# Kernel optimization log

Hardware: AMD Instinct MI355X
Metric: run time of the kernel (lower is better)

The kernel has to match this reference:

```python
import jax, jax.numpy as jnp
import numpy as np

B, L, IN_DIM = 4, 1024, 46
D, DS, K, EXP, NL = 256, 64, 4, 2, 4
DI = EXP * D            # 512 d_inner
HD = 64                 # ssm headdim
H = DI // HD            # 8 ssm heads
XBC = DI + 2 * DS       # 640 conv channels
DIP = 2 * DI + 2 * DS + H  # 1160 in_proj out dim
DFF = D * EXP           # 512 GatedMLP hidden
AH = 4                  # attn heads
AHD = D // AH           # 64


def setup_inputs() -> dict:
    key = jax.random.key(0)
    ks = iter(jax.random.split(key, 40))
    def rn(shape, s=0.05):
        return jax.random.normal(next(ks), shape, jnp.float32) * s
    return {
        'x': jax.random.normal(next(ks), (B, L, IN_DIM), jnp.float32),
        'pos_emb': rn((1, L, D), 0.02),
        'in_w': rn((IN_DIM, D)), 'in_b': jnp.zeros((D,), jnp.float32),
        'ln1_w': jnp.ones((NL, D), jnp.float32), 'ln1_b': jnp.zeros((NL, D), jnp.float32),
        'ssm_in_w': rn((NL, D, DIP)),
        'ssm_conv_w': rn((NL, K, XBC), 0.1), 'ssm_conv_b': jnp.zeros((NL, XBC), jnp.float32),
        'ssm_dt_bias': jnp.full((NL, H), -4.0, jnp.float32),
        'ssm_A_log': jnp.log(jnp.tile(jnp.arange(1.0, H + 1.0), (NL, 1))).astype(jnp.float32),
        'ssm_D': jnp.ones((NL, H), jnp.float32),
        'ssm_norm_w': jnp.ones((NL, DI), jnp.float32),
        'ssm_out_w': rn((NL, DI, D)),
        'ln2_w': jnp.ones((NL, D), jnp.float32), 'ln2_b': jnp.zeros((NL, D), jnp.float32),
        'fc1_w': rn((NL, D, 2 * DFF)), 'fc1_b': jnp.zeros((NL, 2 * DFF), jnp.float32),
        'fc2_w': rn((NL, DFF, D)), 'fc2_b': jnp.zeros((NL, D), jnp.float32),
        'attn_ln_w': jnp.ones((2, D), jnp.float32), 'attn_ln_b': jnp.zeros((2, D), jnp.float32),
        'attn_qkv_w': rn((2, D, 3 * D)), 'attn_qkv_b': jnp.zeros((2, 3 * D), jnp.float32),
        'attn_out_w': rn((2, D, D)), 'attn_out_b': jnp.zeros((2, D), jnp.float32),
        'norm_w': jnp.ones((D,), jnp.float32), 'norm_b': jnp.zeros((D,), jnp.float32),
        'dir_w': rn((D, 3)), 'dir_b': jnp.zeros((3,), jnp.float32),
        'reg_w': rn((D, 3)), 'reg_b': jnp.zeros((3,), jnp.float32),
    }


def _ln(x, w, b, eps=1e-5):
    m = jnp.mean(x, -1, keepdims=True)
    v = jnp.mean(jnp.square(x - m), -1, keepdims=True)
    return (x - m) * jax.lax.rsqrt(v + eps) * w + b


def _mamba2(h, in_w, conv_w, conv_b, dt_bias, A_log, Dh, nw, out_w):
    Bb, Ls, _ = h.shape
    zxbcdt = h @ in_w                               # [B,L,1160]
    z = zxbcdt[..., :DI]
    xBC = zxbcdt[..., DI:DI + XBC]
    dt = zxbcdt[..., DI + XBC:]                     # [B,L,H]
    # causal depthwise conv1d, kernel K
    xp = jnp.pad(xBC, ((0, 0), (K - 1, 0), (0, 0)))
    xBC = sum(xp[:, k:k + Ls, :] * conv_w[k] for k in range(K)) + conv_b
    xBC = jax.nn.silu(xBC)
    xs = xBC[..., :DI]
    Bm = xBC[..., DI:DI + DS]                       # [B,L,N]
    Cm = xBC[..., DI + DS:]                         # [B,L,N]
    dt = jax.nn.softplus(dt + dt_bias)              # [B,L,H]
    a = dt * (-jnp.exp(A_log))                      # [B,L,H], log-decay per step
    cA = jnp.cumsum(a, axis=1).transpose(0, 2, 1)   # [B,H,L]
    diff = cA[:, :, :, None] - cA[:, :, None, :]    # [B,H,L,L]
    mask = jnp.tril(jnp.ones((Ls, Ls), bool))
    decay = jnp.exp(jnp.where(mask, diff, -jnp.inf))
    CB = jnp.einsum('btn,bsn->bts', Cm, Bm)         # [B,L,L]
    S = decay * CB[:, None] * dt.transpose(0, 2, 1)[:, :, None, :]  # [B,H,L,L]
    x4 = xs.reshape(Bb, Ls, H, HD)
    y = jnp.einsum('bhts,bshp->bthp', S, x4) + Dh[None, None, :, None] * x4
    y = y.reshape(Bb, Ls, DI)
    y = y * jax.nn.silu(z)                          # gated
    y = y * jax.lax.rsqrt(jnp.mean(y * y, -1, keepdims=True) + 1e-5) * nw  # RMSNorm
    return y @ out_w


def _attn(h, qkv_w, qkv_b, out_w, out_b):
    Bb, Ls, _ = h.shape
    qkv = h @ qkv_w + qkv_b
    q, k, v = jnp.split(qkv, 3, axis=-1)
    q = q.reshape(Bb, Ls, AH, AHD).transpose(0, 2, 1, 3)
    k = k.reshape(Bb, Ls, AH, AHD).transpose(0, 2, 1, 3)
    v = v.reshape(Bb, Ls, AH, AHD).transpose(0, 2, 1, 3)
    scores = jnp.einsum('bhtd,bhsd->bhts', q, k) / np.sqrt(AHD).astype(np.float32)
    p = jax.nn.softmax(scores, axis=-1)
    o = jnp.einsum('bhts,bhsd->bhtd', p, v).transpose(0, 2, 1, 3).reshape(Bb, Ls, D)
    return o @ out_w + out_b


def _gmlp(h, w1, b1, w2, b2):
    x1, x2 = jnp.split(h @ w1 + b1, 2, axis=-1)
    return (jax.nn.gelu(x1, approximate=False) * x2) @ w2 + b2


def _forward(x, pos_emb, in_w, in_b, ln1_w, ln1_b, ssm_in_w, ssm_conv_w, ssm_conv_b,
             ssm_dt_bias, ssm_A_log, ssm_D, ssm_norm_w, ssm_out_w, ln2_w, ln2_b,
             fc1_w, fc1_b, fc2_w, fc2_b, attn_ln_w, attn_ln_b, attn_qkv_w, attn_qkv_b,
             attn_out_w, attn_out_b, norm_w, norm_b, dir_w, dir_b, reg_w, reg_b):
    Ls = x.shape[1]
    h = x @ in_w + in_b + pos_emb[:, :Ls, :]
    for i in range(NL):
        h = h + _mamba2(_ln(h, ln1_w[i], ln1_b[i]), ssm_in_w[i], ssm_conv_w[i],
                        ssm_conv_b[i], ssm_dt_bias[i], ssm_A_log[i], ssm_D[i],
                        ssm_norm_w[i], ssm_out_w[i])
        if i % 2 == 1:
            j = i // 2
            h = h + _attn(_ln(h, attn_ln_w[j], attn_ln_b[j]), attn_qkv_w[j],
                          attn_qkv_b[j], attn_out_w[j], attn_out_b[j])
        h = h + _gmlp(_ln(h, ln2_w[i], ln2_b[i]), fc1_w[i], fc1_b[i], fc2_w[i], fc2_b[i])
    h = _ln(h, norm_w, norm_b)
    hm = jnp.mean(h, axis=1)                        # [B, D]
    return hm @ dir_w + dir_b, hm @ reg_w + reg_b


def reference(x, pos_emb, in_w, in_b, ln1_w, ln1_b, ssm_in_w, ssm_conv_w, ssm_conv_b,
              ssm_dt_bias, ssm_A_log, ssm_D, ssm_norm_w, ssm_out_w, ln2_w, ln2_b,
              fc1_w, fc1_b, fc2_w, fc2_b, attn_ln_w, attn_ln_b, attn_qkv_w, attn_qkv_b,
              attn_out_w, attn_out_b, norm_w, norm_b, dir_w, dir_b, reg_w, reg_b):
    return _forward(x, pos_emb, in_w, in_b, ln1_w, ln1_b, ssm_in_w, ssm_conv_w,
                    ssm_conv_b, ssm_dt_bias, ssm_A_log, ssm_D, ssm_norm_w, ssm_out_w,
                    ln2_w, ln2_b, fc1_w, fc1_b, fc2_w, fc2_b, attn_ln_w, attn_ln_b,
                    attn_qkv_w, attn_qkv_b, attn_out_w, attn_out_b, norm_w, norm_b,
                    dir_w, dir_b, reg_w, reg_b)
```

## Files before the change

### kernel.cpp

```cpp
#include <hip/hip_runtime.h>
#include <math.h>

#define B_ 4
#define L_ 1024
#define IN_DIM_ 46
#define D_ 256
#define DS_ 64
#define K_ 4
#define NL_ 4
#define DI_ 512
#define HD_ 64
#define H_ 8
#define XBC_ 640
#define DIP_ 1160
#define DFF_ 512
#define AH_ 4
#define AHD_ 64
#define NT_ (B_*L_)
#define QKVD_ (3*D_)

__device__ __forceinline__ float block_sum_256(float v) {
    __shared__ float sb[4];
    #pragma unroll
    for (int off = 32; off > 0; off >>= 1) v += __shfl_down(v, off, 64);
    int lane = threadIdx.x & 63, wid = threadIdx.x >> 6;
    if (lane == 0) sb[wid] = v;
    __syncthreads();
    float r = sb[0] + sb[1] + sb[2] + sb[3];
    __syncthreads();
    return r;
}

__device__ __forceinline__ float siluf(float x) { return x / (1.f + expf(-x)); }
__device__ __forceinline__ float softplusf(float x) {
    return (x > 20.f) ? x : log1pf(expf(x));
}

__global__ __launch_bounds__(256) void in_proj_kernel(
        const float* __restrict__ x, const float* __restrict__ in_w,
        const float* __restrict__ in_b, const float* __restrict__ pos,
        float* __restrict__ Hb) {
    int t = blockIdx.x, tid = threadIdx.x;
    int l = t % L_;
    __shared__ float xs[IN_DIM_];
    if (tid < IN_DIM_) xs[tid] = x[(size_t)t * IN_DIM_ + tid];
    __syncthreads();
    float acc = in_b[tid] + pos[(size_t)l * D_ + tid];
    #pragma unroll 2
    for (int c = 0; c < IN_DIM_; ++c) acc += xs[c] * in_w[c * D_ + tid];
    Hb[(size_t)t * D_ + tid] = acc;
}

__global__ __launch_bounds__(256) void ln_kernel(
        const float* __restrict__ in, const float* __restrict__ w,
        const float* __restrict__ b, float* __restrict__ out) {
    int r = blockIdx.x, tid = threadIdx.x;
    float v = in[(size_t)r * D_ + tid];
    float mean = block_sum_256(v) * (1.f / D_);
    float c = v - mean;
    float var = block_sum_256(c * c) * (1.f / D_);
    out[(size_t)r * D_ + tid] = c * rsqrtf(var + 1e-5f) * w[tid] + b[tid];
}

template<bool BIAS, bool RES>
__global__ __launch_bounds__(256) void gemm64(
        const float* __restrict__ A, const float* __restrict__ W,
        const float* __restrict__ bias, const float* __restrict__ res,
        float* __restrict__ C, int M, int N, int Kd) {
    __shared__ __align__(16) float As[32][68];
    __shared__ __align__(16) float Ws[32][68];
    int tid = threadIdx.x;
    int tx = tid & 15, ty = tid >> 4;
    int n0 = blockIdx.x * 64, m0 = blockIdx.y * 64;
    float acc[4][4] = {};
    for (int k0 = 0; k0 < Kd; k0 += 32) {
        {
            int k = tid & 31, m = tid >> 5;
            #pragma unroll
            for (int i = 0; i < 8; ++i)
                As[k][m + i * 8] = A[(size_t)(m0 + m + i * 8) * Kd + k0 + k];
        }
        {
            #pragma unroll
            for (int i = 0; i < 2; ++i) {
                int idx = tid + i * 256;
                int k = idx >> 4, nq = idx & 15;
                int n = n0 + nq * 4;
                float4 wv;
                if (n + 3 < N) {
                    wv = *(const float4*)&W[(size_t)(k0 + k) * N + n];
                } else {
                    wv.x = (n + 0 < N) ? W[(size_t)(k0 + k) * N + n + 0] : 0.f;
                    wv.y = (n + 1 < N) ? W[(size_t)(k0 + k) * N + n + 1] : 0.f;
                    wv.z = (n + 2 < N) ? W[(size_t)(k0 + k) * N + n + 2] : 0.f;
                    wv.w = (n + 3 < N) ? W[(size_t)(k0 + k) * N + n + 3] : 0.f;
                }
                *(float4*)&Ws[k][nq * 4] = wv;
            }
        }
        __syncthreads();
        #pragma unroll
        for (int k = 0; k < 32; ++k) {
            float4 a  = *(const float4*)&As[k][ty * 4];
            float4 bb = *(const float4*)&Ws[k][tx * 4];
            acc[0][0] += a.x * bb.x; acc[0][1] += a.x * bb.y; acc[0][2] += a.x * bb.z; acc[0][3] += a.x * bb.w;
            acc[1][0] += a.y * bb.x; acc[1][1] += a.y * bb.y; acc[1][2] += a.y * bb.z; acc[1][3] += a.y * bb.w;
            acc[2][0] += a.z * bb.x; acc[2][1] += a.z * bb.y; acc[2][2] += a.z * bb.z; acc[2][3] += a.z * bb.w;
            acc[3][0] += a.w * bb.x; acc[3][1] += a.w * bb.y; acc[3][2] += a.w * bb.z; acc[3][3] += a.w * bb.w;
        }
        __syncthreads();
    }
    #pragma unroll
    for (int i = 0; i < 4; ++i) {
        int m = m0 + ty * 4 + i;
        int n = n0 + tx * 4;
        if (n + 3 < N) {
            float4 v = {acc[i][0], acc[i][1], acc[i][2], acc[i][3]};
            if (BIAS) {
                float4 bv = *(const float4*)&bias[n];
                v.x += bv.x; v.y += bv.y; v.z += bv.z; v.w += bv.w;
            }
            if (RES) {
                float4 rv = *(const float4*)&res[(size_t)m * N + n];
                v.x += rv.x; v.y += rv.y; v.z += rv.z; v.w += rv.w;
            }
            *(float4*)&C[(size_t)m * N + n] = v;
        } else {
            #pragma unroll
            for (int j = 0; j < 4; ++j) {
                int nn = n + j;
                if (nn < N) {
                    float v = acc[i][j];
                    if (BIAS) v += bias[nn];
                    if (RES) v += res[(size_t)m * N + nn];
                    C[(size_t)m * N + nn] = v;
                }
            }
        }
    }
}

__global__ __launch_bounds__(256) void conv_kernel(
        const float* __restrict__ ZX, const float* __restrict__ cw,
        const float* __restrict__ cb, float* __restrict__ XC) {
    int idx = blockIdx.x * 256 + threadIdx.x;
    if (idx >= NT_ * XBC_) return;
    int c = idx % XBC_;
    int t = idx / XBC_;
    int l = t % L_;
    float acc = cb[c];
    #pragma unroll
    for (int k = 0; k < K_; ++k) {
        int lp = l + k - (K_ - 1);
        if (lp >= 0)
            acc += ZX[(size_t)(t + k - (K_ - 1)) * DIP_ + DI_ + c] * cw[k * XBC_ + c];
    }
    XC[(size_t)idx] = siluf(acc);
}

__global__ __launch_bounds__(256) void dt_cumsum_kernel(
        const float* __restrict__ ZX, const float* __restrict__ dt_bias,
        const float* __restrict__ A_log, float* __restrict__ DT,
        float* __restrict__ CA) {
    int b = blockIdx.x / H_, h = blockIdx.x % H_;
    int tid = threadIdx.x;
    __shared__ float sc[256];
    float nA = -expf(A_log[h]);
    float bias = dt_bias[h];
    float carry = 0.f;
    for (int chunk = 0; chunk < L_ / 256; ++chunk) {
        int l = chunk * 256 + tid;
        size_t t = (size_t)b * L_ + l;
        float xv = ZX[t * DIP_ + DI_ + XBC_ + h] + bias;
        float dts = softplusf(xv);
        DT[t * H_ + h] = dts;
        float a = dts * nA;
        sc[tid] = a;
        __syncthreads();
        float v = a;
        for (int off = 1; off < 256; off <<= 1) {
            float add = (tid >= off) ? sc[tid - off] : 0.f;
            __syncthreads();
            v += add;
            sc[tid] = v;
            __syncthreads();
        }
        CA[t * H_ + h] = carry + v;
        carry += sc[255];
        __syncthreads();
    }
}

__global__ __launch_bounds__(256) void cb_kernel(
        const float* __restrict__ XC, float* __restrict__ CB) {
    int b = blockIdx.z;
    int t0 = blockIdx.y * 64, s0 = blockIdx.x * 64;
    if (s0 > t0 + 63) return;
    __shared__ __align__(16) float Cst[64][68];
    __shared__ __align__(16) float Bst[64][68];
    int tid = threadIdx.x, tx = tid & 15, ty = tid >> 4;
    {
        int dq = tid & 15, rr = tid >> 4;
        #pragma unroll
        for (int i = 0; i < 4; ++i) {
            int r2 = rr + i * 16;
            float4 cv = *(const float4*)&XC[(size_t)(b * L_ + t0 + r2) * XBC_ + DI_ + DS_ + dq * 4];
            Cst[dq * 4 + 0][r2] = cv.x; Cst[dq * 4 + 1][r2] = cv.y;
            Cst[dq * 4 + 2][r2] = cv.z; Cst[dq * 4 + 3][r2] = cv.w;
            float4 bv = *(const float4*)&XC[(size_t)(b * L_ + s0 + r2) * XBC_ + DI_ + dq * 4];
            Bst[dq * 4 + 0][r2] = bv.x; Bst[dq * 4 + 1][r2] = bv.y;
            Bst[dq * 4 + 2][r2] = bv.z; Bst[dq * 4 + 3][r2] = bv.w;
        }
    }
    __syncthreads();
    float acc[4][4] = {};
    #pragma unroll 4
    for (int n = 0; n < 64; ++n) {
        float4 a  = *(const float4*)&Cst[n][ty * 4];
        float4 bb = *(const float4*)&Bst[n][tx * 4];
        acc[0][0] += a.x * bb.x; acc[0][1] += a.x * bb.y; acc[0][2] += a.x * bb.z; acc[0][3] += a.x * bb.w;
        acc[1][0] += a.y * bb.x; acc[1][1] += a.y * bb.y; acc[1][2] += a.y * bb.z; acc[1][3] += a.y * bb.w;
        acc[2][0] += a.z * bb.x; acc[2][1] += a.z * bb.y; acc[2][2] += a.z * bb.z; acc[2][3] += a.z * bb.w;
        acc[3][0] += a.w * bb.x; acc[3][1] += a.w * bb.y; acc[3][2] += a.w * bb.z; acc[3][3] += a.w * bb.w;
    }
    #pragma unroll
    for (int i = 0; i < 4; ++i) {
        int t = t0 + ty * 4 + i;
        float4 v = {acc[i][0], acc[i][1], acc[i][2], acc[i][3]};
        *(float4*)&CB[((size_t)b * L_ + t) * L_ + s0 + tx * 4] = v;
    }
}

__global__ __launch_bounds__(256) void ssm_quad_kernel(
        const float* __restrict__ XC, const float* __restrict__ CB,
        const float* __restrict__ DT, const float* __restrict__ CA,
        const float* __restrict__ Dh_ptr, float* __restrict__ Y) {
    int b = blockIdx.z, h = blockIdx.y;
    int t0 = blockIdx.x * 64;
    int tid = threadIdx.x, tx = tid & 15, ty = tid >> 4;
    __shared__ __align__(16) float Pt[64][68];
    __shared__ __align__(16) float Xs[64][68];
    __shared__ float cat[64], cas[64], dts[64];
    if (tid < 64) cat[tid] = CA[((size_t)b * L_ + t0 + tid) * H_ + h];
    float acc[4][4] = {};
    float Dh = Dh_ptr[h];
    for (int s0 = 0; s0 <= t0; s0 += 64) {
        {
            int dq = tid & 15, rr = tid >> 4;
            #pragma unroll
            for (int i = 0; i < 4; ++i) {
                int ss = rr + i * 16;
                *(float4*)&Xs[ss][dq * 4] =
                    *(const float4*)&XC[(size_t)(b * L_ + s0 + ss) * XBC_ + h * HD_ + dq * 4];
            }
        }
        if (tid < 64) {
            cas[tid] = CA[((size_t)b * L_ + s0 + tid) * H_ + h];
            dts[tid] = DT[((size_t)b * L_ + s0 + tid) * H_ + h];
        }
        __syncthreads();
        bool diag = (s0 == t0);
        float p[4][4];
        #pragma unroll
        for (int i = 0; i < 4; ++i) {
            int t = ty * 4 + i;
            float ct = cat[t];
            float4 cbv = *(const float4*)&CB[((size_t)b * L_ + t0 + t) * L_ + s0 + tx * 4];
            float cb4[4] = {cbv.x, cbv.y, cbv.z, cbv.w};
            #pragma unroll
            for (int j = 0; j < 4; ++j) {
                int s = tx * 4 + j;
                float v = expf(ct - cas[s]) * cb4[j] * dts[s];
                if (diag && s > t) v = 0.f;
                p[i][j] = v;
            }
        }
        #pragma unroll
        for (int j = 0; j < 4; ++j) {
            float4 col = {p[0][j], p[1][j], p[2][j], p[3][j]};
            *(float4*)&Pt[tx * 4 + j][ty * 4] = col;
        }
        __syncthreads();
        #pragma unroll 4
        for (int s = 0; s < 64; ++s) {
            float4 a  = *(const float4*)&Pt[s][ty * 4];
            float4 xv = *(const float4*)&Xs[s][tx * 4];
            acc[0][0] += a.x * xv.x; acc[0][1] += a.x * xv.y; acc[0][2] += a.x * xv.z; acc[0][3] += a.x * xv.w;
            acc[1][0] += a.y * xv.x; acc[1][1] += a.y * xv.y; acc[1][2] += a.y * xv.z; acc[1][3] += a.y * xv.w;
            acc[2][0] += a.z * xv.x; acc[2][1] += a.z * xv.y; acc[2][2] += a.z * xv.z; acc[2][3] += a.z * xv.w;
            acc[3][0] += a.w * xv.x; acc[3][1] += a.w * xv.y; acc[3][2] += a.w * xv.z; acc[3][3] += a.w * xv.w;
        }
        __syncthreads();
    }
    #pragma unroll
    for (int i = 0; i < 4; ++i) {
        size_t t = (size_t)b * L_ + t0 + ty * 4 + i;
        float4 x4 = *(const float4*)&XC[t * XBC_ + h * HD_ + tx * 4];
        float4 o = {acc[i][0] + Dh * x4.x, acc[i][1] + Dh * x4.y,
                    acc[i][2] + Dh * x4.z, acc[i][3] + Dh * x4.w};
        *(float4*)&Y[t * DI_ + h * HD_ + tx * 4] = o;
    }
}

__global__ __launch_bounds__(256) void gate_rms_kernel(
        float* __restrict__ Y, const float* __restrict__ ZX,
        const float* __restrict__ nw) {
    int r = blockIdx.x, tid = threadIdx.x;
    size_t ry = (size_t)r * DI_, rz = (size_t)r * DIP_;
    float y0 = Y[ry + tid], y1 = Y[ry + 256 + tid];
    float z0 = ZX[rz + tid], z1 = ZX[rz + 256 + tid];
    y0 *= siluf(z0);
    y1 *= siluf(z1);
    float ss = block_sum_256(y0 * y0 + y1 * y1) * (1.f / DI_);
    float s = rsqrtf(ss + 1e-5f);
    Y[ry + tid] = y0 * s * nw[tid];
    Y[ry + 256 + tid] = y1 * s * nw[256 + tid];
}

__global__ __launch_bounds__(256) void attn_kernel(
        const float* __restrict__ QKV, float* __restrict__ O) {
    int b = blockIdx.z, hh = blockIdx.y;
    int t0 = blockIdx.x * 32;
    int tid = threadIdx.x, tx = tid & 15, ty = tid >> 4;
    __shared__ __align__(16) float Qt[64][34];
    __shared__ __align__(16) float Kt[64][68];
    __shared__ __align__(16) float Vs[64][68];
    __shared__ __align__(16) float Pt[64][34];
    {
        int dq = tid & 15, r = tid >> 4;
        #pragma unroll
        for (int i = 0; i < 2; ++i) {
            int rr = r + i * 16;
            float4 v = *(const float4*)&QKV[(size_t)(b * L_ + t0 + rr) * QKVD_ + hh * AHD_ + dq * 4];
            Qt[dq * 4 + 0][rr] = v.x * 0.125f;
            Qt[dq * 4 + 1][rr] = v.y * 0.125f;
            Qt[dq * 4 + 2][rr] = v.z * 0.125f;
            Qt[dq * 4 + 3][rr] = v.w * 0.125f;
        }
    }
    float m[2], l[2], acc[2][4] = {};
    m[0] = m[1] = -INFINITY; l[0] = l[1] = 0.f;
    for (int s0 = 0; s0 < L_; s0 += 64) {
        {
            int dq = tid & 15, s = tid >> 4;
            #pragma unroll
            for (int i = 0; i < 4; ++i) {
                int ss = s + i * 16;
                float4 kv = *(const float4*)&QKV[(size_t)(b * L_ + s0 + ss) * QKVD_ + D_ + hh * AHD_ + dq * 4];
                Kt[dq * 4 + 0][ss] = kv.x; Kt[dq * 4 + 1][ss] = kv.y;
                Kt[dq * 4 + 2][ss] = kv.z; Kt[dq * 4 + 3][ss] = kv.w;
                *(float4*)&Vs[ss][dq * 4] =
                    *(const float4*)&QKV[(size_t)(b * L_ + s0 + ss) * QKVD_ + 2 * D_ + hh * AHD_ + dq * 4];
            }
        }
        __syncthreads();
        float sv[2][4] = {};
        #pragma unroll 8
        for (int d = 0; d < 64; ++d) {
            float2 a  = *(const float2*)&Qt[d][ty * 2];
            float4 kk = *(const float4*)&Kt[d][tx * 4];
            sv[0][0] += a.x * kk.x; sv[0][1] += a.x * kk.y; sv[0][2] += a.x * kk.z; sv[0][3] += a.x * kk.w;
            sv[1][0] += a.y * kk.x; sv[1][1] += a.y * kk.y; sv[1][2] += a.y * kk.z; sv[1][3] += a.y * kk.w;
        }
        #pragma unroll
        for (int i = 0; i < 2; ++i) {
            float mx = fmaxf(fmaxf(sv[i][0], sv[i][1]), fmaxf(sv[i][2], sv[i][3]));
            #pragma unroll
            for (int o = 1; o < 16; o <<= 1) mx = fmaxf(mx, __shfl_xor(mx, o, 64));
            float nm = fmaxf(m[i], mx);
            float corr = expf(m[i] - nm);
            m[i] = nm;
            float sum = 0.f;
            #pragma unroll
            for (int j = 0; j < 4; ++j) { sv[i][j] = expf(sv[i][j] - nm); sum += sv[i][j]; }
            #pragma unroll
            for (int o = 1; o < 16; o <<= 1) sum += __shfl_xor(sum, o, 64);
            l[i] = l[i] * corr + sum;
            #pragma unroll
            for (int j = 0; j < 4; ++j) acc[i][j] *= corr;
        }
        #pragma unroll
        for (int j = 0; j < 4; ++j) {
            float2 pp = {sv[0][j], sv[1][j]};
            *(float2*)&Pt[tx * 4 + j][ty * 2] = pp;
        }
        __syncthreads();
        #pragma unroll 8
        for (int s = 0; s < 64; ++s) {
            float2 pp = *(const float2*)&Pt[s][ty * 2];
            float4 vv = *(const float4*)&Vs[s][tx * 4];
            acc[0][0] += pp.x * vv.x; acc[0][1] += pp.x * vv.y; acc[0][2] += pp.x * vv.z; acc[0][3] += pp.x * vv.w;
            acc[1][0] += pp.y * vv.x; acc[1][1] += pp.y * vv.y; acc[1][2] += pp.y * vv.z; acc[1][3] += pp.y * vv.w;
        }
        __syncthreads();
    }
    #pragma unroll
    for (int i = 0; i < 2; ++i) {
        float inv = 1.f / l[i];
        size_t t = (size_t)b * L_ + t0 + ty * 2 + i;
        float4 o = {acc[i][0] * inv, acc[i][1] * inv, acc[i][2] * inv, acc[i][3] * inv};
        *(float4*)&O[t * D_ + hh * AHD_ + tx * 4] = o;
    }
}

__global__ __launch_bounds__(256) void geglu_kernel(
        const float* __restrict__ M1, float* __restrict__ M2) {
    int idx = blockIdx.x * 256 + threadIdx.x;
    if (idx >= NT_ * DFF_) return;
    int r = idx / DFF_, c = idx % DFF_;
    float x1 = M1[(size_t)r * (2 * DFF_) + c];
    float x2 = M1[(size_t)r * (2 * DFF_) + DFF_ + c];
    float g = 0.5f * x1 * (1.f + erff(x1 * 0.70710678118f));
    M2[(size_t)idx] = g * x2;
}

__global__ __launch_bounds__(256) void head_partial_kernel(
        const float* __restrict__ LN, float* __restrict__ part) {
    int chunk = blockIdx.x, b = blockIdx.y;
    int tid = threadIdx.x;
    float s = 0.f;
    for (int l = 0; l < 64; ++l)
        s += LN[(size_t)(b * L_ + chunk * 64 + l) * D_ + tid];
    part[(size_t)(b * 16 + chunk) * D_ + tid] = s;
}

__global__ __launch_bounds__(256) void head_final_kernel(
        const float* __restrict__ part, const float* __restrict__ dir_w,
        const float* __restrict__ dir_b, const float* __restrict__ reg_w,
        const float* __restrict__ reg_b, float* __restrict__ out) {
    int b = blockIdx.x, tid = threadIdx.x;
    __shared__ float hm[256];
    float s = 0.f;
// ... 38 lines not shown
    const float* fc2_b      = (const float*)d_in[19];
    const float* attn_ln_w  = (const float*)d_in[20];
    const float* attn_ln_b  = (const float*)d_in[21];
    const float* attn_qkv_w = (const float*)d_in[22];
    const float* attn_qkv_b = (const float*)d_in[23];
    const float* attn_out_w = (const float*)d_in[24];
    const float* attn_out_b = (const float*)d_in[25];
    const float* norm_w     = (const float*)d_in[26];
    const float* norm_b     = (const float*)d_in[27];
    const float* dir_w      = (const float*)d_in[28];
    const float* dir_b      = (const float*)d_in[29];
    const float* reg_w      = (const float*)d_in[30];
    const float* reg_b      = (const float*)d_in[31];
    float* out = (float*)d_out;
    float* ws  = (float*)d_ws;

    size_t off = 0;
    float* Hb  = ws + off; off += (size_t)NT_ * D_;
    float* LN  = ws + off; off += (size_t)NT_ * D_;
    float* ZX  = ws + off; off += (size_t)NT_ * DIP_;
    float* XC  = ws + off; off += (size_t)NT_ * XBC_;
    float* DTb = ws + off; off += (size_t)NT_ * H_;
    float* CAb = ws + off; off += (size_t)NT_ * H_;
    float* CBb = ws + off; off += (size_t)B_ * L_ * L_;
    float* Yb  = ws + off; off += (size_t)NT_ * DI_;
    float* HP  = ws + off; off += (size_t)B_ * 16 * D_;

    dim3 blk(256);

    in_proj_kernel<<<NT_, blk, 0, stream>>>(x, in_w, in_b, pos_emb, Hb);

    for (int i = 0; i < NL_; ++i) {
        ln_kernel<<<NT_, blk, 0, stream>>>(Hb, ln1_w + i * D_, ln1_b + i * D_, LN);
        gemm64<false,false><<<dim3(cdiv(DIP_,64), NT_/64), blk, 0, stream>>>(
            LN, ssm_in_w + (size_t)i * D_ * DIP_, nullptr, nullptr, ZX, NT_, DIP_, D_);
        conv_kernel<<<cdiv(NT_*XBC_,256), blk, 0, stream>>>(
            ZX, ssm_conv_w + (size_t)i * K_ * XBC_, ssm_conv_b + i * XBC_, XC);
        dt_cumsum_kernel<<<B_*H_, blk, 0, stream>>>(
            ZX, ssm_dt_bias + i * H_, ssm_A_log + i * H_, DTb, CAb);
        cb_kernel<<<dim3(L_/64, L_/64, B_), blk, 0, stream>>>(XC, CBb);
        ssm_quad_kernel<<<dim3(L_/64, H_, B_), blk, 0, stream>>>(
            XC, CBb, DTb, CAb, ssm_Dp + i * H_, Yb);
        gate_rms_kernel<<<NT_, blk, 0, stream>>>(Yb, ZX, ssm_norm_w + (size_t)i * DI_);
        gemm64<false,true><<<dim3(cdiv(D_,64), NT_/64), blk, 0, stream>>>(
            Yb, ssm_out_w + (size_t)i * DI_ * D_, nullptr, Hb, Hb, NT_, D_, DI_);

        if (i % 2 == 1) {
            int j = i / 2;
            ln_kernel<<<NT_, blk, 0, stream>>>(Hb, attn_ln_w + j * D_, attn_ln_b + j * D_, LN);
            gemm64<true,false><<<dim3(cdiv(QKVD_,64), NT_/64), blk, 0, stream>>>(
                LN, attn_qkv_w + (size_t)j * D_ * QKVD_, attn_qkv_b + j * QKVD_,
                nullptr, ZX, NT_, QKVD_, D_);
            attn_kernel<<<dim3(L_/32, AH_, B_), blk, 0, stream>>>(ZX, XC);
            gemm64<true,true><<<dim3(cdiv(D_,64), NT_/64), blk, 0, stream>>>(
                XC, attn_out_w + (size_t)j * D_ * D_, attn_out_b + j * D_,
                Hb, Hb, NT_, D_, D_);
        }

        ln_kernel<<<NT_, blk, 0, stream>>>(Hb, ln2_w + i * D_, ln2_b + i * D_, LN);
        gemm64<true,false><<<dim3(cdiv(2*DFF_,64), NT_/64), blk, 0, stream>>>(
            LN, fc1_w + (size_t)i * D_ * 2 * DFF_, fc1_b + i * 2 * DFF_,
            nullptr, ZX, NT_, 2 * DFF_, D_);
        geglu_kernel<<<cdiv(NT_*DFF_,256), blk, 0, stream>>>(ZX, XC);
        gemm64<true,true><<<dim3(cdiv(D_,64), NT_/64), blk, 0, stream>>>(
            XC, fc2_w + (size_t)i * DFF_ * D_, fc2_b + i * D_,
            Hb, Hb, NT_, D_, DFF_);
    }

    ln_kernel<<<NT_, blk, 0, stream>>>(Hb, norm_w, norm_b, LN);
    head_partial_kernel<<<dim3(16, B_), blk, 0, stream>>>(LN, HP);
    head_final_kernel<<<B_, blk, 0, stream>>>(HP, dir_w, dir_b, reg_w, reg_b, out);
}
```

Before: 1.562 ms.

## Add 128x128 GEMM tile, widen attention query tile, warp-scan dt cumsum

Adds a gemm128 kernel in which each thread computes an 8x8 output block, and uses it for the wide in_proj and fc1 GEMMs to raise arithmetic intensity per shared-memory load. The attention kernel now processes 64 queries per block instead of 32, each thread owning four query rows, and the P tile is stored with an XOR swizzle to avoid shared-memory bank conflicts. The dt cumsum replaces its shared-memory Hillis-Steele scan, which synchronises on every step, with wavefront shuffle scans plus one cross-wave combine. Larger tiles use more registers and launch fewer blocks, which may lower occupancy and leave some compute units idle.

Measured after the change: 1.661 ms. +6.3%, slower.

```diff
diff --git a/kernel.cpp b/kernel.cpp
--- a/kernel.cpp
+++ b/kernel.cpp
@@ -36,6 +36,13 @@
     return (x > 20.f) ? x : log1pf(expf(x));
 }
 
+__device__ __forceinline__ void fma44(float (&c)[4][4], float4 a, float4 b) {
+    c[0][0] += a.x*b.x; c[0][1] += a.x*b.y; c[0][2] += a.x*b.z; c[0][3] += a.x*b.w;
+    c[1][0] += a.y*b.x; c[1][1] += a.y*b.y; c[1][2] += a.y*b.z; c[1][3] += a.y*b.w;
+    c[2][0] += a.z*b.x; c[2][1] += a.z*b.y; c[2][2] += a.z*b.z; c[2][3] += a.z*b.w;
+    c[3][0] += a.w*b.x; c[3][1] += a.w*b.y; c[3][2] += a.w*b.z; c[3][3] += a.w*b.w;
+}
+
 __global__ __launch_bounds__(256) void in_proj_kernel(
         const float* __restrict__ x, const float* __restrict__ in_w,
         const float* __restrict__ in_b, const float* __restrict__ pos,
@@ -103,10 +110,7 @@
         for (int k = 0; k < 32; ++k) {
             float4 a  = *(const float4*)&As[k][ty * 4];
             float4 bb = *(const float4*)&Ws[k][tx * 4];
-            acc[0][0] += a.x * bb.x; acc[0][1] += a.x * bb.y; acc[0][2] += a.x * bb.z; acc[0][3] += a.x * bb.w;
-            acc[1][0] += a.y * bb.x; acc[1][1] += a.y * bb.y; acc[1][2] += a.y * bb.z; acc[1][3] += a.y * bb.w;
-            acc[2][0] += a.z * bb.x; acc[2][1] += a.z * bb.y; acc[2][2] += a.z * bb.z; acc[2][3] += a.z * bb.w;
-            acc[3][0] += a.w * bb.x; acc[3][1] += a.w * bb.y; acc[3][2] += a.w * bb.z; acc[3][3] += a.w * bb.w;
+            fma44(acc, a, bb);
         }
         __syncthreads();
     }
@@ -134,6 +138,101 @@
                     if (BIAS) v += bias[nn];
                     if (RES) v += res[(size_t)m * N + nn];
                     C[(size_t)m * N + nn] = v;
+                }
+            }
+        }
+    }
+}
+
+template<bool BIAS, bool RES>
+__global__ __launch_bounds__(256) void gemm128(
+        const float* __restrict__ A, const float* __restrict__ W,
+        const float* __restrict__ bias, const float* __restrict__ res,
+        float* __restrict__ C, int M, int N, int Kd) {
+    __shared__ __align__(16) float As[32][132];
+    __shared__ __align__(16) float Ws[32][132];
+    int tid = threadIdx.x;
+    int tx = tid & 15, ty = tid >> 4;
+    int n0 = blockIdx.x * 128, m0 = blockIdx.y * 128;
+    int am = tid >> 1;
+    int ak = (tid & 1) * 16;
+    int wk = tid >> 3;
+    int wn = (tid & 7) * 16;
+    float acc[2][2][4][4] = {};
+    for (int k0 = 0; k0 < Kd; k0 += 32) {
+        {
+            const float* Ap = &A[(size_t)(m0 + am) * Kd + k0 + ak];
+            #pragma unroll
+            for (int q = 0; q < 4; ++q) {
+                float4 av = *(const float4*)&Ap[q * 4];
+                As[ak + q * 4 + 0][am] = av.x;
+                As[ak + q * 4 + 1][am] = av.y;
+                As[ak + q * 4 + 2][am] = av.z;
+                As[ak + q * 4 + 3][am] = av.w;
+            }
+        }
+        {
+            const float* Wp = &W[(size_t)(k0 + wk) * N + n0 + wn];
+            #pragma unroll
+            for (int q = 0; q < 4; ++q) {
+                int n = n0 + wn + q * 4;
+                float4 wv;
+                if (n + 3 < N) {
+                    wv = *(const float4*)&Wp[q * 4];
+                } else {
+                    wv.x = (n + 0 < N) ? Wp[q * 4 + 0] : 0.f;
+                    wv.y = (n + 1 < N) ? Wp[q * 4 + 1] : 0.f;
+                    wv.z = (n + 2 < N) ? Wp[q * 4 + 2] : 0.f;
+                    wv.w = (n + 3 < N) ? Wp[q * 4 + 3] : 0.f;
+                }
+                *(float4*)&Ws[wk][wn + q * 4] = wv;
+            }
+        }
+        __syncthreads();
+        #pragma unroll
+        for (int k = 0; k < 32; ++k) {
+            float4 a0 = *(const float4*)&As[k][ty * 4];
+            float4 a1 = *(const float4*)&As[k][64 + ty * 4];
+            float4 w0 = *(const float4*)&Ws[k][tx * 4];
+            float4 w1 = *(const float4*)&Ws[k][64 + tx * 4];
+            fma44(acc[0][0], a0, w0);
+            fma44(acc[0][1], a0, w1);
+            fma44(acc[1][0], a1, w0);
+            fma44(acc[1][1], a1, w1);
+        }
+        __syncthreads();
+    }
+    #pragma unroll
+    for (int rh = 0; rh < 2; ++rh) {
+        #pragma unroll
+        for (int i = 0; i < 4; ++i) {
+            int m = m0 + rh * 64 + ty * 4 + i;
+            #pragma unroll
+            for (int ch = 0; ch < 2; ++ch) {
+                int n = n0 + ch * 64 + tx * 4;
+                if (n + 3 < N) {
+                    float4 v = {acc[rh][ch][i][0], acc[rh][ch][i][1],
+                                acc[rh][ch][i][2], acc[rh][ch][i][3]};
+                    if (BIAS) {
+                        float4 bv = *(const float4*)&bias[n];
+                        v.x += bv.x; v.y += bv.y; v.z += bv.z; v.w += bv.w;
+                    }
+                    if (RES) {
+                        float4 rv = *(const float4*)&res[(size_t)m * N + n];
+                        v.x += rv.x; v.y += rv.y; v.z += rv.z; v.w += rv.w;
+                    }
+                    *(float4*)&C[(size_t)m * N + n] = v;
+                } else {
+                    #pragma unroll
+                    for (int j = 0; j < 4; ++j) {
+                        int nn = n + j;
+                        if (nn < N) {
+                            float v = acc[rh][ch][i][j];
+                            if (BIAS) v += bias[nn];
+                            if (RES) v += res[(size_t)m * N + nn];
+                            C[(size_t)m * N + nn] = v;
+                        }
+                    }
                 }
             }
         }
@@ -163,31 +262,33 @@
         const float* __restrict__ A_log, float* __restrict__ DT,
         float* __restrict__ CA) {
     int b = blockIdx.x / H_, h = blockIdx.x % H_;
-    int tid = threadIdx.x;
-    __shared__ float sc[256];
+    int tid = threadIdx.x, lane = tid & 63, wid = tid >> 6;
+    __shared__ float wsum[4];
     float nA = -expf(A_log[h]);
     float bias = dt_bias[h];
     float carry = 0.f;
+    #pragma unroll
     for (int chunk = 0; chunk < L_ / 256; ++chunk) {
         int l = chunk * 256 + tid;
         size_t t = (size_t)b * L_ + l;
-        float xv = ZX[t * DIP_ + DI_ + XBC_ + h] + bias;
-        float dts = softplusf(xv);
+        float dts = softplusf(ZX[t * DIP_ + DI_ + XBC_ + h] + bias);
         DT[t * H_ + h] = dts;
-        float a = dts * nA;
-        sc[tid] = a;
-        __syncthreads();
-        float v = a;
-        for (int off = 1; off < 256; off <<= 1) {
-            float add = (tid >= off) ? sc[tid - off] : 0.f;
-            __syncthreads();
-            v += add;
-            sc[tid] = v;
-            __syncthreads();
-        }
-        CA[t * H_ + h] = carry + v;
-        carry += sc[255];
-        __syncthreads();
+        float v = dts * nA;
+        #pragma unroll
+        for (int o = 1; o < 64; o <<= 1) {
+            float u = __shfl_up(v, o, 64);
+            if (lane >= o) v += u;
+        }
+        if (lane == 63) wsum[wid] = v;
+        __syncthreads();
+        float pre = carry;
+        if (wid > 0) pre += wsum[0];
+        if (wid > 1) pre += wsum[1];
+        if (wid > 2) pre += wsum[2];
+        float tot = wsum[0] + wsum[1] + wsum[2] + wsum[3];
+        __syncthreads();
+        CA[t * H_ + h] = pre + v;
+        carry += tot;
     }
 }
 
@@ -218,10 +319,7 @@
     for (int n = 0; n < 64; ++n) {
         float4 a  = *(const float4*)&Cst[n][ty * 4];
         float4 bb = *(const float4*)&Bst[n][tx * 4];
-        acc[0][0] += a.x * bb.x; acc[0][1] += a.x * bb.y; acc[0][2] += a.x * bb.z; acc[0][3] += a.x * bb.w;
-        acc[1][0] += a.y * bb.x; acc[1][1] += a.y * bb.y; acc[1][2] += a.y * bb.z; acc[1][3] += a.y * bb.w;
-        acc[2][0] += a.z * bb.x; acc[2][1] += a.z * bb.y; acc[2][2] += a.z * bb.z; acc[2][3] += a.z * bb.w;
-        acc[3][0] += a.w * bb.x; acc[3][1] += a.w * bb.y; acc[3][2] += a.w * bb.z; acc[3][3] += a.w * bb.w;
+        fma44(acc, a, bb);
     }
     #pragma unroll
     for (int i = 0; i < 4; ++i) {
@@ -285,10 +383,7 @@
         for (int s = 0; s < 64; ++s) {
             float4 a  = *(const float4*)&Pt[s][ty * 4];
             float4 xv = *(const float4*)&Xs[s][tx * 4];
-            acc[0][0] += a.x * xv.x; acc[0][1] += a.x * xv.y; acc[0][2] += a.x * xv.z; acc[0][3] += a.x * xv.w;
-            acc[1][0] += a.y * xv.x; acc[1][1] += a.y * xv.y; acc[1][2] += a.y * xv.z; acc[1][3] += a.y * xv.w;
-            acc[2][0] += a.z * xv.x; acc[2][1] += a.z * xv.y; acc[2][2] += a.z * xv.z; acc[2][3] += a.z * xv.w;
-            acc[3][0] += a.w * xv.x; acc[3][1] += a.w * xv.y; acc[3][2] += a.w * xv.z; acc[3][3] += a.w * xv.w;
+            fma44(acc, a, xv);
         }
         __syncthreads();
     }
@@ -320,16 +415,16 @@
 __global__ __launch_bounds__(256) void attn_kernel(
         const float* __restrict__ QKV, float* __restrict__ O) {
     int b = blockIdx.z, hh = blockIdx.y;
-    int t0 = blockIdx.x * 32;
+    int t0 = blockIdx.x * 64;
     int tid = threadIdx.x, tx = tid & 15, ty = tid >> 4;
-    __shared__ __align__(16) float Qt[64][34];
+    __shared__ __align__(16) float Qt[64][68];
     __shared__ __align__(16) float Kt[64][68];
     __shared__ __align__(16) float Vs[64][68];
-    __shared__ __align__(16) float Pt[64][34];
+    __shared__ __align__(16) float Pt[64][68];
     {
         int dq = tid & 15, r = tid >> 4;
         #pragma unroll
-        for (int i = 0; i < 2; ++i) {
+        for (int i = 0; i < 4; ++i) {
             int rr = r + i * 16;
             float4 v = *(const float4*)&QKV[(size_t)(b * L_ + t0 + rr) * QKVD_ + hh * AHD_ + dq * 4];
             Qt[dq * 4 + 0][rr] = v.x * 0.125f;
@@ -338,8 +433,9 @@
             Qt[dq * 4 + 3][rr] = v.w * 0.125f;
         }
     }
-    float m[2], l[2], acc[2][4] = {};
-    m[0] = m[1] = -INFINITY; l[0] = l[1] = 0.f;
+    float m[4], l[4], acc[4][4] = {};
+    #pragma unroll
+    for (int i = 0; i < 4; ++i) { m[i] = -INFINITY; l[i] = 0.f; }
     for (int s0 = 0; s0 < L_; s0 += 64) {
         {
             int dq = tid & 15, s = tid >> 4;
@@ -354,16 +450,15 @@
             }
         }
         __syncthreads();
-        float sv[2][4] = {};
-        #pragma unroll 8
+        float sv[4][4] = {};
+        #pragma unroll 4
         for (int d = 0; d < 64; ++d) {
-            float2 a  = *(const float2*)&Qt[d][ty * 2];
+            float4 a  = *(const float4*)&Qt[d][ty * 4];
             float4 kk = *(const float4*)&Kt[d][tx * 4];
-            sv[0][0] += a.x * kk.x; sv[0][1] += a.x * kk.y; sv[0][2] += a.x * kk.z; sv[0][3] += a.x * kk.w;
-            sv[1][0] += a.y * kk.x; sv[1][1] += a.y * kk.y; sv[1][2] += a.y * kk.z; sv[1][3] += a.y * kk.w;
-        }
-        #pragma unroll
-        for (int i = 0; i < 2; ++i) {
+            fma44(sv, a, kk);
+        }
+        #pragma unroll
+        for (int i = 0; i < 4; ++i) {
             float mx = fmaxf(fmaxf(sv[i][0], sv[i][1]), fmaxf(sv[i][2], sv[i][3]));
             #pragma unroll
             for (int o = 1; o < 16; o <<= 1) mx = fmaxf(mx, __shfl_xor(mx, o, 64));
@@ -379,25 +474,27 @@
             #pragma unroll
             for (int j = 0; j < 4; ++j) acc[i][j] *= corr;
         }
-        #pragma unroll
-        for (int j = 0; j < 4; ++j) {
-            float2 pp = {sv[0][j], sv[1][j]};
-            *(float2*)&Pt[tx * 4 + j][ty * 2] = pp;
-        }
-        __syncthreads();
-        #pragma unroll 8
+        {
+            int cg = ((ty ^ tx) & 15) * 4;
+            #pragma unroll
+            for (int j = 0; j < 4; ++j) {
+                float4 col = {sv[0][j], sv[1][j], sv[2][j], sv[3][j]};
+                *(float4*)&Pt[tx * 4 + j][cg] = col;
+            }
+        }
+        __syncthreads();
+        #pragma unroll 4
         for (int s = 0; s < 64; ++s) {
-            float2 pp = *(const float2*)&Pt[s][ty * 2];
+            float4 pp = *(const float4*)&Pt[s][((ty ^ (s >> 2)) & 15) * 4];
             float4 vv = *(const float4*)&Vs[s][tx * 4];
-            acc[0][0] += pp.x * vv.x; acc[0][1] += pp.x * vv.y; acc[0][2] += pp.x * vv.z; acc[0][3] += pp.x * vv.w;
-            acc[1][0] += pp.y * vv.x; acc[1][1] += pp.y * vv.y; acc[1][2] += pp.y * vv.z; acc[1][3] += pp.y * vv.w;
-        }
-        __syncthreads();
-    }
-    #pragma unroll
-    for (int i = 0; i < 2; ++i) {
+            fma44(acc, pp, vv);
+        }
+        __syncthreads();
+    }
+    #pragma unroll
+    for (int i = 0; i < 4; ++i) {
         float inv = 1.f / l[i];
-        size_t t = (size_t)b * L_ + t0 + ty * 2 + i;
+        size_t t = (size_t)b * L_ + t0 + ty * 4 + i;
         float4 o = {acc[i][0] * inv, acc[i][1] * inv, acc[i][2] * inv, acc[i][3] * inv};
         *(float4*)&O[t * D_ + hh * AHD_ + tx * 4] = o;
     }
@@ -502,7 +599,7 @@
 
     for (int i = 0; i < NL_; ++i) {
         ln_kernel<<<NT_, blk, 0, stream>>>(Hb, ln1_w + i * D_, ln1_b + i * D_, LN);
-        gemm64<false,false><<<dim3(cdiv(DIP_,64), NT_/64), blk, 0, stream>>>(
+        gemm128<false,false><<<dim3(cdiv(DIP_,128), NT_/128), blk, 0, stream>>>(
             LN, ssm_in_w + (size_t)i * D_ * DIP_, nullptr, nullptr, ZX, NT_, DIP_, D_);
         conv_kernel<<<cdiv(NT_*XBC_,256), blk, 0, stream>>>(
             ZX, ssm_conv_w + (size_t)i * K_ * XBC_, ssm_conv_b + i * XBC_, XC);
@@ -521,14 +618,14 @@
             gemm64<true,false><<<dim3(cdiv(QKVD_,64), NT_/64), blk, 0, stream>>>(
                 LN, attn_qkv_w + (size_t)j * D_ * QKVD_, attn_qkv_b + j * QKVD_,
                 nullptr, ZX, NT_, QKVD_, D_);
-            attn_kernel<<<dim3(L_/32, AH_, B_), blk, 0, stream>>>(ZX, XC);
+            attn_kernel<<<dim3(L_/64, AH_, B_), blk, 0, stream>>>(ZX, XC);
             gemm64<true,true><<<dim3(cdiv(D_,64), NT_/64), blk, 0, stream>>>(
                 XC, attn_out_w + (size_t)j * D_ * D_, attn_out_b + j * D_,
                 Hb, Hb, NT_, D_, D_);
         }
 
         ln_kernel<<<NT_, blk, 0, stream>>>(Hb, ln2_w + i * D_, ln2_b + i * D_, LN);
-        gemm64<true,false><<<dim3(cdiv(2*DFF_,64), NT_/64), blk, 0, stream>>>(
+        gemm128<true,false><<<dim3(cdiv(2*DFF_,128), NT_/128), blk, 0, stream>>>(
             LN, fc1_w + (size_t)i * D_ * 2 * DFF_, fc1_b + i * 2 * DFF_,
             nullptr, ZX, NT_, 2 * DFF_, D_);
         geglu_kernel<<<cdiv(NT_*DFF_,256), blk, 0, stream>>>(ZX, XC);
```

## Read GEMM/SSM/attention B operands from global directly, warp-shuffle scan, larger attn tiles

Applied to the files above, without the earlier changes.

The GEMM no longer stages the weight tile in shared memory. Each thread reads its float4 weight columns straight from global/L1, and the ssm_quad and attention kernels do the same for X and V. The dt cumsum switches from a shared-memory Hillis-Steele scan to wavefront shuffle scans with a per-wave carry. Attention now processes 64 query rows per block with a 4x4 register tile and an XOR-swizzled P buffer. These changes cut LDS traffic and barriers, but they make the inner loops depend on global/L1 latency and bandwidth rather than LDS reuse.

Measured after the change: 2.769 ms. 1.77x slower.

```diff
diff --git a/kernel.cpp b/kernel.cpp
--- a/kernel.cpp
+++ b/kernel.cpp
@@ -36,6 +36,13 @@
     return (x > 20.f) ? x : log1pf(expf(x));
 }
 
+__device__ __forceinline__ void fma44(float (&c)[4][4], float4 a, float4 b) {
+    c[0][0] += a.x*b.x; c[0][1] += a.x*b.y; c[0][2] += a.x*b.z; c[0][3] += a.x*b.w;
+    c[1][0] += a.y*b.x; c[1][1] += a.y*b.y; c[1][2] += a.y*b.z; c[1][3] += a.y*b.w;
+    c[2][0] += a.z*b.x; c[2][1] += a.z*b.y; c[2][2] += a.z*b.z; c[2][3] += a.z*b.w;
+    c[3][0] += a.w*b.x; c[3][1] += a.w*b.y; c[3][2] += a.w*b.z; c[3][3] += a.w*b.w;
+}
+
 __global__ __launch_bounds__(256) void in_proj_kernel(
         const float* __restrict__ x, const float* __restrict__ in_w,
         const float* __restrict__ in_b, const float* __restrict__ pos,
@@ -63,15 +70,16 @@
 }
 
 template<bool BIAS, bool RES>
-__global__ __launch_bounds__(256) void gemm64(
+__global__ __launch_bounds__(256) void gemm_bd(
         const float* __restrict__ A, const float* __restrict__ W,
         const float* __restrict__ bias, const float* __restrict__ res,
         float* __restrict__ C, int M, int N, int Kd) {
     __shared__ __align__(16) float As[32][68];
-    __shared__ __align__(16) float Ws[32][68];
     int tid = threadIdx.x;
     int tx = tid & 15, ty = tid >> 4;
     int n0 = blockIdx.x * 64, m0 = blockIdx.y * 64;
+    int n = n0 + tx * 4;
+    bool nfull = (n + 3 < N);
     float acc[4][4] = {};
     for (int k0 = 0; k0 < Kd; k0 += 32) {
         {
@@ -80,41 +88,39 @@
             for (int i = 0; i < 8; ++i)
                 As[k][m + i * 8] = A[(size_t)(m0 + m + i * 8) * Kd + k0 + k];
         }
-        {
-            #pragma unroll
-            for (int i = 0; i < 2; ++i) {
-                int idx = tid + i * 256;
-                int k = idx >> 4, nq = idx & 15;
-                int n = n0 + nq * 4;
-                float4 wv;
-                if (n + 3 < N) {
-                    wv = *(const float4*)&W[(size_t)(k0 + k) * N + n];
-                } else {
-                    wv.x = (n + 0 < N) ? W[(size_t)(k0 + k) * N + n + 0] : 0.f;
-                    wv.y = (n + 1 < N) ? W[(size_t)(k0 + k) * N + n + 1] : 0.f;
-                    wv.z = (n + 2 < N) ? W[(size_t)(k0 + k) * N + n + 2] : 0.f;
-                    wv.w = (n + 3 < N) ? W[(size_t)(k0 + k) * N + n + 3] : 0.f;
+        __syncthreads();
+        if (nfull) {
+            #pragma unroll
+            for (int kc = 0; kc < 4; ++kc) {
+                float4 bb[8];
+                #pragma unroll
+                for (int u = 0; u < 8; ++u)
+                    bb[u] = *(const float4*)&W[(size_t)(k0 + kc * 8 + u) * N + n];
+                #pragma unroll
+                for (int u = 0; u < 8; ++u) {
+                    float4 a = *(const float4*)&As[kc * 8 + u][ty * 4];
+                    fma44(acc, a, bb[u]);
                 }
-                *(float4*)&Ws[k][nq * 4] = wv;
-            }
-        }
-        __syncthreads();
-        #pragma unroll
-        for (int k = 0; k < 32; ++k) {
-            float4 a  = *(const float4*)&As[k][ty * 4];
-            float4 bb = *(const float4*)&Ws[k][tx * 4];
-            acc[0][0] += a.x * bb.x; acc[0][1] += a.x * bb.y; acc[0][2] += a.x * bb.z; acc[0][3] += a.x * bb.w;
-            acc[1][0] += a.y * bb.x; acc[1][1] += a.y * bb.y; acc[1][2] += a.y * bb.z; acc[1][3] += a.y * bb.w;
-            acc[2][0] += a.z * bb.x; acc[2][1] += a.z * bb.y; acc[2][2] += a.z * bb.z; acc[2][3] += a.z * bb.w;
-            acc[3][0] += a.w * bb.x; acc[3][1] += a.w * bb.y; acc[3][2] += a.w * bb.z; acc[3][3] += a.w * bb.w;
+            }
+        } else {
+            #pragma unroll 8
+            for (int k = 0; k < 32; ++k) {
+                const float* wr = &W[(size_t)(k0 + k) * N];
+                float4 bb;
+                bb.x = (n + 0 < N) ? wr[n + 0] : 0.f;
+                bb.y = (n + 1 < N) ? wr[n + 1] : 0.f;
+                bb.z = (n + 2 < N) ? wr[n + 2] : 0.f;
+                bb.w = (n + 3 < N) ? wr[n + 3] : 0.f;
+                float4 a = *(const float4*)&As[k][ty * 4];
+                fma44(acc, a, bb);
+            }
         }
         __syncthreads();
     }
     #pragma unroll
     for (int i = 0; i < 4; ++i) {
         int m = m0 + ty * 4 + i;
-        int n = n0 + tx * 4;
-        if (n + 3 < N) {
+        if (nfull) {
             float4 v = {acc[i][0], acc[i][1], acc[i][2], acc[i][3]};
             if (BIAS) {
                 float4 bv = *(const float4*)&bias[n];
@@ -163,31 +169,33 @@
         const float* __restrict__ A_log, float* __restrict__ DT,
         float* __restrict__ CA) {
     int b = blockIdx.x / H_, h = blockIdx.x % H_;
-    int tid = threadIdx.x;
-    __shared__ float sc[256];
+    int tid = threadIdx.x, lane = tid & 63, wid = tid >> 6;
+    __shared__ float wsum[4];
     float nA = -expf(A_log[h]);
     float bias = dt_bias[h];
     float carry = 0.f;
+    #pragma unroll
     for (int chunk = 0; chunk < L_ / 256; ++chunk) {
         int l = chunk * 256 + tid;
         size_t t = (size_t)b * L_ + l;
-        float xv = ZX[t * DIP_ + DI_ + XBC_ + h] + bias;
-        float dts = softplusf(xv);
+        float dts = softplusf(ZX[t * DIP_ + DI_ + XBC_ + h] + bias);
         DT[t * H_ + h] = dts;
-        float a = dts * nA;
-        sc[tid] = a;
-        __syncthreads();
-        float v = a;
-        for (int off = 1; off < 256; off <<= 1) {
-            float add = (tid >= off) ? sc[tid - off] : 0.f;
-            __syncthreads();
-            v += add;
-            sc[tid] = v;
-            __syncthreads();
-        }
-        CA[t * H_ + h] = carry + v;
-        carry += sc[255];
-        __syncthreads();
+        float v = dts * nA;
+        #pragma unroll
+        for (int o = 1; o < 64; o <<= 1) {
+            float u = __shfl_up(v, o, 64);
+            if (lane >= o) v += u;
+        }
+        if (lane == 63) wsum[wid] = v;
+        __syncthreads();
+        float pre = carry;
+        if (wid > 0) pre += wsum[0];
+        if (wid > 1) pre += wsum[1];
+        if (wid > 2) pre += wsum[2];
+        float tot = wsum[0] + wsum[1] + wsum[2] + wsum[3];
+        __syncthreads();
+        CA[t * H_ + h] = pre + v;
+        carry += tot;
     }
 }
 
@@ -218,10 +226,7 @@
     for (int n = 0; n < 64; ++n) {
         float4 a  = *(const float4*)&Cst[n][ty * 4];
         float4 bb = *(const float4*)&Bst[n][tx * 4];
-        acc[0][0] += a.x * bb.x; acc[0][1] += a.x * bb.y; acc[0][2] += a.x * bb.z; acc[0][3] += a.x * bb.w;
-        acc[1][0] += a.y * bb.x; acc[1][1] += a.y * bb.y; acc[1][2] += a.y * bb.z; acc[1][3] += a.y * bb.w;
-        acc[2][0] += a.z * bb.x; acc[2][1] += a.z * bb.y; acc[2][2] += a.z * bb.z; acc[2][3] += a.z * bb.w;
-        acc[3][0] += a.w * bb.x; acc[3][1] += a.w * bb.y; acc[3][2] += a.w * bb.z; acc[3][3] += a.w * bb.w;
+        fma44(acc, a, bb);
     }
     #pragma unroll
     for (int i = 0; i < 4; ++i) {
@@ -239,21 +244,11 @@
     int t0 = blockIdx.x * 64;
     int tid = threadIdx.x, tx = tid & 15, ty = tid >> 4;
     __shared__ __align__(16) float Pt[64][68];
-    __shared__ __align__(16) float Xs[64][68];
     __shared__ float cat[64], cas[64], dts[64];
     if (tid < 64) cat[tid] = CA[((size_t)b * L_ + t0 + tid) * H_ + h];
     float acc[4][4] = {};
     float Dh = Dh_ptr[h];
     for (int s0 = 0; s0 <= t0; s0 += 64) {
-        {
-            int dq = tid & 15, rr = tid >> 4;
-            #pragma unroll
-            for (int i = 0; i < 4; ++i) {
-                int ss = rr + i * 16;
-                *(float4*)&Xs[ss][dq * 4] =
-                    *(const float4*)&XC[(size_t)(b * L_ + s0 + ss) * XBC_ + h * HD_ + dq * 4];
-            }
-        }
         if (tid < 64) {
             cas[tid] = CA[((size_t)b * L_ + s0 + tid) * H_ + h];
             dts[tid] = DT[((size_t)b * L_ + s0 + tid) * H_ + h];
@@ -284,11 +279,8 @@
         #pragma unroll 4
         for (int s = 0; s < 64; ++s) {
             float4 a  = *(const float4*)&Pt[s][ty * 4];
-            float4 xv = *(const float4*)&Xs[s][tx * 4];
-            acc[0][0] += a.x * xv.x; acc[0][1] += a.x * xv.y; acc[0][2] += a.x * xv.z; acc[0][3] += a.x * xv.w;
-            acc[1][0] += a.y * xv.x; acc[1][1] += a.y * xv.y; acc[1][2] += a.y * xv.z; acc[1][3] += a.y * xv.w;
-            acc[2][0] += a.z * xv.x; acc[2][1] += a.z * xv.y; acc[2][2] += a.z * xv.z; acc[2][3] += a.z * xv.w;
-            acc[3][0] += a.w * xv.x; acc[3][1] += a.w * xv.y; acc[3][2] += a.w * xv.z; acc[3][3] += a.w * xv.w;
+            float4 xv = *(const float4*)&XC[(size_t)(b * L_ + s0 + s) * XBC_ + h * HD_ + tx * 4];
+            fma44(acc, a, xv);
         }
         __syncthreads();
     }
@@ -320,16 +312,15 @@
 __global__ __launch_bounds__(256) void attn_kernel(
         const float* __restrict__ QKV, float* __restrict__ O) {
     int b = blockIdx.z, hh = blockIdx.y;
-    int t0 = blockIdx.x * 32;
+    int t0 = blockIdx.x * 64;
     int tid = threadIdx.x, tx = tid & 15, ty = tid >> 4;
-    __shared__ __align__(16) float Qt[64][34];
+    __shared__ __align__(16) float Qt[64][68];
     __shared__ __align__(16) float Kt[64][68];
-    __shared__ __align__(16) float Vs[64][68];
-    __shared__ __align__(16) float Pt[64][34];
+    __shared__ __align__(16) float Pt[64][68];
     {
         int dq = tid & 15, r = tid >> 4;
         #pragma unroll
-        for (int i = 0; i < 2; ++i) {
+        for (int i = 0; i < 4; ++i) {
             int rr = r + i * 16;
             float4 v = *(const float4*)&QKV[(size_t)(b * L_ + t0 + rr) * QKVD_ + hh * AHD_ + dq * 4];
             Qt[dq * 4 + 0][rr] = v.x * 0.125f;
@@ -338,8 +329,9 @@
             Qt[dq * 4 + 3][rr] = v.w * 0.125f;
         }
     }
-    float m[2], l[2], acc[2][4] = {};
-    m[0] = m[1] = -INFINITY; l[0] = l[1] = 0.f;
+    float m[4], l[4], acc[4][4] = {};
+    #pragma unroll
+    for (int i = 0; i < 4; ++i) { m[i] = -INFINITY; l[i] = 0.f; }
     for (int s0 = 0; s0 < L_; s0 += 64) {
         {
             int dq = tid & 15, s = tid >> 4;
@@ -349,21 +341,18 @@
                 float4 kv = *(const float4*)&QKV[(size_t)(b * L_ + s0 + ss) * QKVD_ + D_ + hh * AHD_ + dq * 4];
                 Kt[dq * 4 + 0][ss] = kv.x; Kt[dq * 4 + 1][ss] = kv.y;
                 Kt[dq * 4 + 2][ss] = kv.z; Kt[dq * 4 + 3][ss] = kv.w;
-                *(float4*)&Vs[ss][dq * 4] =
-                    *(const float4*)&QKV[(size_t)(b * L_ + s0 + ss) * QKVD_ + 2 * D_ + hh * AHD_ + dq * 4];
-            }
-        }
-        __syncthreads();
-        float sv[2][4] = {};
-        #pragma unroll 8
+            }
+        }
+        __syncthreads();
+        float sv[4][4] = {};
+        #pragma unroll 4
         for (int d = 0; d < 64; ++d) {
-            float2 a  = *(const float2*)&Qt[d][ty * 2];
+            float4 a  = *(const float4*)&Qt[d][ty * 4];
             float4 kk = *(const float4*)&Kt[d][tx * 4];
-            sv[0][0] += a.x * kk.x; sv[0][1] += a.x * kk.y; sv[0][2] += a.x * kk.z; sv[0][3] += a.x * kk.w;
-            sv[1][0] += a.y * kk.x; sv[1][1] += a.y * kk.y; sv[1][2] += a.y * kk.z; sv[1][3] += a.y * kk.w;
+            fma44(sv, a, kk);
         }
         #pragma unroll
-        for (int i = 0; i < 2; ++i) {
+        for (int i = 0; i < 4; ++i) {
             float mx = fmaxf(fmaxf(sv[i][0], sv[i][1]), fmaxf(sv[i][2], sv[i][3]));
             #pragma unroll
             for (int o = 1; o < 16; o <<= 1) mx = fmaxf(mx, __shfl_xor(mx, o, 64));
@@ -379,25 +368,27 @@
             #pragma unroll
             for (int j = 0; j < 4; ++j) acc[i][j] *= corr;
         }
-        #pragma unroll
-        for (int j = 0; j < 4; ++j) {
-            float2 pp = {sv[0][j], sv[1][j]};
-            *(float2*)&Pt[tx * 4 + j][ty * 2] = pp;
-        }
-        __syncthreads();
-        #pragma unroll 8
+        {
+            int cg = ((ty ^ tx) & 15) * 4;
+            #pragma unroll
+            for (int j = 0; j < 4; ++j) {
+                float4 col = {sv[0][j], sv[1][j], sv[2][j], sv[3][j]};
+                *(float4*)&Pt[tx * 4 + j][cg] = col;
+            }
+        }
+        __syncthreads();
+        #pragma unroll 4
         for (int s = 0; s < 64; ++s) {
-            float2 pp = *(const float2*)&Pt[s][ty * 2];
-            float4 vv = *(const float4*)&Vs[s][tx * 4];
-            acc[0][0] += pp.x * vv.x; acc[0][1] += pp.x * vv.y; acc[0][2] += pp.x * vv.z; acc[0][3] += pp.x * vv.w;
-            acc[1][0] += pp.y * vv.x; acc[1][1] += pp.y * vv.y; acc[1][2] += pp.y * vv.z; acc[1][3] += pp.y * vv.w;
-        }
-        __syncthreads();
-    }
-    #pragma unroll
-    for (int i = 0; i < 2; ++i) {
+            float4 pp = *(const float4*)&Pt[s][((ty ^ (s >> 2)) & 15) * 4];
+            float4 vv = *(const float4*)&QKV[(size_t)(b * L_ + s0 + s) * QKVD_ + 2 * D_ + hh * AHD_ + tx * 4];
+            fma44(acc, pp, vv);
+        }
+        __syncthreads();
+    }
+    #pragma unroll
+    for (int i = 0; i < 4; ++i) {
         float inv = 1.f / l[i];
-        size_t t = (size_t)b * L_ + t0 + ty * 2 + i;
+        size_t t = (size_t)b * L_ + t0 + ty * 4 + i;
         float4 o = {acc[i][0] * inv, acc[i][1] * inv, acc[i][2] * inv, acc[i][3] * inv};
         *(float4*)&O[t * D_ + hh * AHD_ + tx * 4] = o;
     }
@@ -502,7 +493,7 @@
 
     for (int i = 0; i < NL_; ++i) {
         ln_kernel<<<NT_, blk, 0, stream>>>(Hb, ln1_w + i * D_, ln1_b + i * D_, LN);
-        gemm64<false,false><<<dim3(cdiv(DIP_,64), NT_/64), blk, 0, stream>>>(
+        gemm_bd<false,false><<<dim3(cdiv(DIP_,64), NT_/64), blk, 0, stream>>>(
             LN, ssm_in_w + (size_t)i * D_ * DIP_, nullptr, nullptr, ZX, NT_, DIP_, D_);
         conv_kernel<<<cdiv(NT_*XBC_,256), blk, 0, stream>>>(
             ZX, ssm_conv_w + (size_t)i * K_ * XBC_, ssm_conv_b + i * XBC_, XC);
@@ -512,27 +503,27 @@
         ssm_quad_kernel<<<dim3(L_/64, H_, B_), blk, 0, stream>>>(
             XC, CBb, DTb, CAb, ssm_Dp + i * H_, Yb);
         gate_rms_kernel<<<NT_, blk, 0, stream>>>(Yb, ZX, ssm_norm_w + (size_t)i * DI_);
-        gemm64<false,true><<<dim3(cdiv(D_,64), NT_/64), blk, 0, stream>>>(
+        gemm_bd<false,true><<<dim3(cdiv(D_,64), NT_/64), blk, 0, stream>>>(
             Yb, ssm_out_w + (size_t)i * DI_ * D_, nullptr, Hb, Hb, NT_, D_, DI_);
 
         if (i % 2 == 1) {
             int j = i / 2;
             ln_kernel<<<NT_, blk, 0, stream>>>(Hb, attn_ln_w + j * D_, attn_ln_b + j * D_, LN);
-            gemm64<true,false><<<dim3(cdiv(QKVD_,64), NT_/64), blk, 0, stream>>>(
+            gemm_bd<true,false><<<dim3(cdiv(QKVD_,64), NT_/64), blk, 0, stream>>>(
                 LN, attn_qkv_w + (size_t)j * D_ * QKVD_, attn_qkv_b + j * QKVD_,
                 nullptr, ZX, NT_, QKVD_, D_);
-            attn_kernel<<<dim3(L_/32, AH_, B_), blk, 0, stream>>>(ZX, XC);
-            gemm64<true,true><<<dim3(cdiv(D_,64), NT_/64), blk, 0, stream>>>(
+            attn_kernel<<<dim3(L_/64, AH_, B_), blk, 0, stream>>>(ZX, XC);
+            gemm_bd<true,true><<<dim3(cdiv(D_,64), NT_/64), blk, 0, stream>>>(
                 XC, attn_out_w + (size_t)j * D_ * D_, attn_out_b + j * D_,
                 Hb, Hb, NT_, D_, D_);
         }
 
         ln_kernel<<<NT_, blk, 0, stream>>>(Hb, ln2_w + i * D_, ln2_b + i * D_, LN);
-        gemm64<true,false><<<dim3(cdiv(2*DFF_,64), NT_/64), blk, 0, stream>>>(
+        gemm_bd<true,false><<<dim3(cdiv(2*DFF_,64), NT_/64), blk, 0, stream>>>(
             LN, fc1_w + (size_t)i * D_ * 2 * DFF_, fc1_b + i * 2 * DFF_,
             nullptr, ZX, NT_, 2 * DFF_, D_);
         geglu_kernel<<<cdiv(NT_*DFF_,256), blk, 0, stream>>>(ZX, XC);
-        gemm64<true,true><<<dim3(cdiv(D_,64), NT_/64), blk, 0, stream>>>(
+        gemm_bd<true,true><<<dim3(cdiv(D_,64), NT_/64), blk, 0, stream>>>(
             XC, fc2_w + (size_t)i * DFF_ * D_, fc2_b + i * D_,
             Hb, Hb, NT_, D_, DFF_);
     }
```
